# Kernel tuning notes

Hardware: AMD Instinct MI355X
Metric: run time of the kernel (lower is better)

Reference implementation:

```python
import jax, jax.numpy as jnp
import numpy as np

HEADS = 8
RANK = 4

def _lora(x, w_down, w_up, palette, in_dim, out_dim):
    # w_down: [RANK*in_dim, 15], w_up: [RANK*out_dim, 15], palette: [1, 15]
    down = (palette @ w_down.T).reshape(RANK, in_dim)   # [r, in]
    up = (palette @ w_up.T).reshape(out_dim, RANK)      # [out, r]
    return (x @ down.T) @ up.T                          # [..., out]


def setup_inputs() -> dict:
    key = jax.random.key(0)
    ks = jax.random.split(key, 16)
    B, S, D = 2, 2048, 1280
    def n(k, shape, std=0.02):
        return (jax.random.normal(k, shape, dtype=jnp.float32) * std).astype(jnp.float32)
    return {
        'hidden_states': jax.random.normal(ks[0], (B, S, D), dtype=jnp.float32),
        'color_palette': jax.random.uniform(ks[1], (1, 15), dtype=jnp.float32),
        'Wq': n(ks[2], (D, D)), 'Wk': n(ks[3], (D, D)),
        'Wv': n(ks[4], (D, D)), 'Wo': n(ks[5], (D, D)),
        'bo': jnp.zeros((D,), dtype=jnp.float32),
        'q_down': n(ks[6], (RANK * D, 15), 0.25), 'q_up': n(ks[7], (RANK * D, 15)),
        'k_down': n(ks[8], (RANK * D, 15), 0.25), 'k_up': n(ks[9], (RANK * D, 15)),
        'v_down': n(ks[10], (RANK * D, 15), 0.25), 'v_up': n(ks[11], (RANK * D, 15)),
        'o_down': n(ks[12], (RANK * D, 15), 0.25), 'o_up': n(ks[13], (RANK * D, 15)),
    }


def reference(hidden_states, color_palette, Wq, Wk, Wv, Wo, bo,
              q_down, q_up, k_down, k_up, v_down, v_up, o_down, o_up):
    B, S, D = hidden_states.shape
    H = HEADS
    hd = D // H
    scale = 1.0  # LoRA scale
    x = hidden_states
    # LoRA-augmented projections (self-attention: encoder_hidden_states = x)
    q = x @ Wq.T + scale * _lora(x, q_down, q_up, color_palette, D, D)
    k = x @ Wk.T + scale * _lora(x, k_down, k_up, color_palette, D, D)
    v = x @ Wv.T + scale * _lora(x, v_down, v_up, color_palette, D, D)
    # split heads: [B, S, D] -> [B, H, S, hd]
    q = q.reshape(B, S, H, hd).transpose(0, 2, 1, 3)
    k = k.reshape(B, S, H, hd).transpose(0, 2, 1, 3)
    v = v.reshape(B, S, H, hd).transpose(0, 2, 1, 3)
    attn_scale = 1.0 / jnp.sqrt(jnp.asarray(hd, dtype=q.dtype))
    scores = jnp.einsum('bhqd,bhkd->bhqk', q, k) * attn_scale
    probs = jax.nn.softmax(scores, axis=-1)
    out = jnp.einsum('bhqk,bhkd->bhqd', probs, v)
    out = out.transpose(0, 2, 1, 3).reshape(B, S, D)
    out = out @ Wo.T + bo + scale * _lora(out, o_down, o_up, color_palette, D, D)
    return out
```

## Files before the change

### kernel.cpp

```cpp
#include <hip/hip_runtime.h>

typedef unsigned short u16;
typedef unsigned int u32;
typedef __attribute__((ext_vector_type(4))) float floatx4;
typedef __attribute__((ext_vector_type(16))) float floatx16;
typedef __attribute__((ext_vector_type(8))) __bf16 bf16x8;
typedef __attribute__((ext_vector_type(2))) unsigned int u32x2;
typedef __attribute__((ext_vector_type(4))) unsigned int u32x4;

#define MFMA_BF16(a, b, c) __builtin_amdgcn_mfma_f32_16x16x32_bf16((a), (b), (c), 0, 0, 0)
#define MFMA32(a, b, c) __builtin_amdgcn_mfma_f32_32x32x16_bf16((a), (b), (c), 0, 0, 0)

typedef const __attribute__((address_space(1))) void* gas_ptr;
typedef __attribute__((address_space(3))) void* las_ptr;

__device__ __forceinline__ void gll16(const void* g, void* l) {
  __builtin_amdgcn_global_load_lds((gas_ptr)g, (las_ptr)l, 16, 0, 0);
}

__device__ __forceinline__ u16 f2bf(float x) {
  u32 u = __builtin_bit_cast(u32, x);
  u = (u + 0x7fffu + ((u >> 16) & 1u)) >> 16;
  return (u16)u;
}

__device__ __forceinline__ u32 cvtpk(float lo, float hi) {
  u32 r;
  asm("v_cvt_pk_bf16_f32 %0, %1, %2" : "=v"(r) : "v"(lo), "v"(hi));
  return r;
}

__global__ void prep_downup(const float* __restrict__ pal,
                            const float* __restrict__ qd, const float* __restrict__ qu,
                            const float* __restrict__ kd, const float* __restrict__ ku,
                            const float* __restrict__ vd, const float* __restrict__ vu,
                            const float* __restrict__ od, const float* __restrict__ ou,
                            float* __restrict__ down_f, float* __restrict__ up_f) {
  int tid = blockIdx.x * blockDim.x + threadIdx.x;
  int w = tid / 10240;
  int rem = tid - w * 10240;
  const float* dsrc = (w == 0) ? qd : (w == 1) ? kd : (w == 2) ? vd : od;
  const float* usrc = (w == 0) ? qu : (w == 1) ? ku : (w == 2) ? vu : ou;
  bool isdown = rem < 5120;
  int row = isdown ? rem : rem - 5120;
  const float* src = (isdown ? dsrc : usrc) + row * 15;
  float s = 0.f;
#pragma unroll
  for (int p = 0; p < 15; ++p) s += pal[p] * src[p];
  if (isdown) down_f[w * 5120 + row] = s;
  else        up_f[w * 5120 + row] = s;
}

__global__ void build_weff_cvtx(const float* __restrict__ Wq, const float* __restrict__ Wk,
                                const float* __restrict__ Wv, const float* __restrict__ Wo,
                                const float* __restrict__ down_f, const float* __restrict__ up_f,
                                u16* __restrict__ weff_qkv, u16* __restrict__ weff_o,
                                const float4* __restrict__ x, ushort4* __restrict__ xb) {
  if (blockIdx.x >= 25600) {
    int i = (blockIdx.x - 25600) * blockDim.x + threadIdx.x;
    float4 v = x[i];
    ushort4 o;
    o.x = f2bf(v.x); o.y = f2bf(v.y); o.z = f2bf(v.z); o.w = f2bf(v.w);
    xb[i] = o;
    return;
  }
  int tid = blockIdx.x * blockDim.x + threadIdx.x;
  int w = tid / 1638400;
  int rem = tid - w * 1638400;
  int n = rem / 1280;
  int k = rem - n * 1280;
  const float* W = (w == 0) ? Wq : (w == 1) ? Wk : (w == 2) ? Wv : Wo;
  const float* up = up_f + w * 5120 + n * 4;
  const float* dn = down_f + w * 5120 + k;
  float v = W[rem] + up[0] * dn[0] + up[1] * dn[1280] + up[2] * dn[2560] + up[3] * dn[3840];
  u16 hv = f2bf(v);
  if (w < 3) weff_qkv[w * 1638400 + rem] = hv;
  else       weff_o[rem] = hv;
}

__global__ __launch_bounds__(256) void gemm128_qkv(const u16* __restrict__ A, const u16* __restrict__ Bm,
                                                   u16* __restrict__ qb, u16* __restrict__ kb,
                                                   u16* __restrict__ vtb, int K) {
  __shared__ __align__(16) u16 smem[128 * 136];
  u16* lA = smem;
  u16* lB = smem + 8192;
  const int t = threadIdx.x;
  const int lane = t & 63;
  const int l15 = lane & 15, quad = lane >> 4;
  const int wid = t >> 6;
  const int wm = (wid >> 1) * 64;
  const int wn = (wid & 1) * 64;
  const int bm = blockIdx.x * 128;
  const int bn = blockIdx.y * 128;
  floatx4 acc[4][4] = {};

  int soff[4];
#pragma unroll
  for (int i = 0; i < 4; ++i) {
    int c = t + i * 256;
    int row = c >> 3, pos = c & 7;
    soff[i] = row * K + ((pos + row) & 7) * 8;
  }
  int afo[4][2], bfo[4][2];
#pragma unroll
  for (int i = 0; i < 4; ++i) {
#pragma unroll
    for (int ch = 0; ch < 2; ++ch) {
      int ra = wm + i * 16 + l15;
      int rb = wn + i * 16 + l15;
      int kc8 = ch * 4 + quad;
      afo[i][ch] = ra * 64 + ((kc8 - ra) & 7) * 8;
      bfo[i][ch] = rb * 64 + ((kc8 - rb) & 7) * 8;
    }
  }

  const u16* Ab = A + (long)bm * K;
  const u16* Bb = Bm + (long)bn * K;
  const int nkt = K >> 6;

  for (int kt = 0; kt < nkt; ++kt) {
    __syncthreads();
    const int k0 = kt * 64;
#pragma unroll
    for (int i = 0; i < 4; ++i) gll16(Ab + (long)soff[i] + k0, lA + (t + i * 256) * 8);
#pragma unroll
    for (int i = 0; i < 4; ++i) gll16(Bb + (long)soff[i] + k0, lB + (t + i * 256) * 8);
    __syncthreads();
#pragma unroll
    for (int ch = 0; ch < 2; ++ch) {
      bf16x8 af[4], bfr[4];
#pragma unroll
      for (int i = 0; i < 4; ++i) af[i] = *(const bf16x8*)(lA + afo[i][ch]);
#pragma unroll
      for (int i = 0; i < 4; ++i) bfr[i] = *(const bf16x8*)(lB + bfo[i][ch]);
#pragma unroll
      for (int i = 0; i < 4; ++i)
#pragma unroll
        for (int j = 0; j < 4; ++j)
          acc[i][j] = MFMA_BF16(af[i], bfr[j], acc[i][j]);
    }
  }

  if (bn < 2560) {
#pragma unroll
    for (int i = 0; i < 4; ++i) {
#pragma unroll
      for (int j = 0; j < 4; ++j) {
#pragma unroll
        for (int r = 0; r < 4; ++r) {
          int m = bm + wm + i * 16 + quad * 4 + r;
          int n = bn + wn + j * 16 + l15;
          u16 hv = f2bf(acc[i][j][r]);
          if (n < 1280) qb[(long)m * 1280 + n] = hv;
          else          kb[(long)m * 1280 + (n - 1280)] = hv;
        }
      }
    }
  } else {
    __syncthreads();
#pragma unroll
    for (int i = 0; i < 4; ++i)
#pragma unroll
      for (int j = 0; j < 4; ++j)
#pragma unroll
        for (int r = 0; r < 4; ++r) {
          int m_loc = wm + i * 16 + quad * 4 + r;
          int n_loc = wn + j * 16 + l15;
          smem[n_loc * 136 + m_loc] = f2bf(acc[i][j][r]);
        }
    __syncthreads();
    const int b = bm >> 11, sbase = bm & 2047;
    u16* dst = vtb + ((long)(b * 1280 + (bn - 2560))) * 2048 + sbase;
#pragma unroll
    for (int it = 0; it < 8; ++it) {
      int idx = it * 256 + t;
      int n_loc = idx >> 4;
      int m0 = (idx & 15) * 8;
      bf16x8 vv = *(const bf16x8*)(smem + n_loc * 136 + m0);
      *(bf16x8*)(dst + (long)n_loc * 2048 + m0) = vv;
    }
  }
}

__global__ __launch_bounds__(256) void gemm128_o(const u16* __restrict__ A, const u16* __restrict__ Bm,
                                                 float* __restrict__ outf,
                                                 const float* __restrict__ bias, int K) {
  __shared__ __align__(16) u16 lA[128 * 64];
  __shared__ __align__(16) u16 lB[128 * 64];
  const int t = threadIdx.x;
  const int lane = t & 63;
  const int l15 = lane & 15, quad = lane >> 4;
  const int wid = t >> 6;
  const int wm = (wid >> 1) * 64;
  const int wn = (wid & 1) * 64;
  const int bm = blockIdx.x * 128;
  const int bn = blockIdx.y * 128;
  floatx4 acc[4][4] = {};

  int soff[4];
#pragma unroll
  for (int i = 0; i < 4; ++i) {
    int c = t + i * 256;
    int row = c >> 3, pos = c & 7;
    soff[i] = row * K + ((pos + row) & 7) * 8;
  }
  int afo[4][2], bfo[4][2];
#pragma unroll
  for (int i = 0; i < 4; ++i) {
#pragma unroll
    for (int ch = 0; ch < 2; ++ch) {
      int ra = wm + i * 16 + l15;
      int rb = wn + i * 16 + l15;
      int kc8 = ch * 4 + quad;
      afo[i][ch] = ra * 64 + ((kc8 - ra) & 7) * 8;
      bfo[i][ch] = rb * 64 + ((kc8 - rb) & 7) * 8;
    }
  }

  const u16* Ab = A + (long)bm * K;
  const u16* Bb = Bm + (long)bn * K;
  const int nkt = K >> 6;

  for (int kt = 0; kt < nkt; ++kt) {
    __syncthreads();
    const int k0 = kt * 64;
#pragma unroll
    for (int i = 0; i < 4; ++i) gll16(Ab + (long)soff[i] + k0, lA + (t + i * 256) * 8);
#pragma unroll
    for (int i = 0; i < 4; ++i) gll16(Bb + (long)soff[i] + k0, lB + (t + i * 256) * 8);
    __syncthreads();
#pragma unroll
    for (int ch = 0; ch < 2; ++ch) {
      bf16x8 af[4], bfr[4];
#pragma unroll
      for (int i = 0; i < 4; ++i) af[i] = *(const bf16x8*)(lA + afo[i][ch]);
#pragma unroll
      for (int i = 0; i < 4; ++i) bfr[i] = *(const bf16x8*)(lB + bfo[i][ch]);
#pragma unroll
      for (int i = 0; i < 4; ++i)
#pragma unroll
        for (int j = 0; j < 4; ++j)
          acc[i][j] = MFMA_BF16(af[i], bfr[j], acc[i][j]);
    }
  }

#pragma unroll
  for (int i = 0; i < 4; ++i) {
#pragma unroll
    for (int j = 0; j < 4; ++j) {
#pragma unroll
      for (int r = 0; r < 4; ++r) {
        int m = bm + wm + i * 16 + quad * 4 + r;
        int n = bn + wn + j * 16 + l15;
        outf[(long)m * 1280 + n] = acc[i][j][r] + bias[n];
      }
    }
  }
}

__global__ __launch_bounds__(512) void flash_attn(const u16* __restrict__ qb,
                                                  const u16* __restrict__ kb,
                                                  const u16* __restrict__ vtb,
                                                  u16* __restrict__ attn) {
  const int D = 1280, HD = 160;
  __shared__ __align__(16) u16 kv_lds[2][20480];
  const int t = threadIdx.x, lane = t & 63, wid = t >> 6;
  const int l31 = lane & 31, hi = lane >> 5;
  const int rg = wid >> 1, kh = wid & 1;
  const int lflat = blockIdx.y * 16 + blockIdx.x;
  const int vswz = (lflat & 7) * 32 + (lflat >> 3);
  const int qi = vswz & 15, bh = vswz >> 4;
  const int b = bh >> 3, h = bh & 7;
  const int q0 = qi * 128 + rg * 32;
  const float kS = 0.11404582025f;

  bf16x8 aq[10];
  {
    const u16* qg = qb + ((long)(b * 2048 + q0 + l31)) * D + h * HD + hi * 8;
#pragma unroll
    for (int kw = 0; kw < 10; ++kw) aq[kw] = *(const bf16x8*)(qg + kw * 16);
  }

  const u16* sg[5];
  int sadv[5];
#pragma unroll
  for (int i = 0; i < 5; ++i) {
    int c = t + i * 512;
    if (c < 1280) {
      int key = c / 20, pos = c - key * 20;
      int g = pos - (3 * key) % 20;
      if (g < 0) g += 20;
      sg[i] = kb + ((long)(b * 2048 + key)) * D + h * HD + g * 8;
      sadv[i] = 64 * D;
    } else {
      int c2 = c - 1280;
      int vrow = c2 >> 3, swz = c2 & 7;
      int vcol = swz ^ (vrow & 7);
      sg[i] = vtb + ((long)(b * 1280 + h * HD + vrow)) * 2048 + vcol * 8;
      sadv[i] = 64;
    }
  }

  int kfo[10];
  {
    int key = kh * 32 + l31;
    int r3 = (3 * key) % 20;
#pragma unroll
    for (int kw = 0; kw < 10; ++kw) {
      int g = kw * 2 + hi;
      int pos = g + r3;
      if (pos >= 20) pos -= 20;
      kfo[kw] = (key * 20 + pos) * 8;
    }
  }
  int vfo[5][2];
#pragma unroll
  for (int db = 0; db < 5; ++db) {
#pragma unroll
    for (int w = 0; w < 2; ++w) {
      int d = db * 32 + l31;
      int gc = kh * 4 + w * 2 + hi;
      int sw = gc ^ (d & 7);
      vfo[db][w] = 10240 + (d * 8 + sw) * 8;
    }
  }

  float l_sum = 0.f;
  floatx16 o_acc[5] = {};
  bf16x8 paA = {}, paB = {};

  gll16(sg[0], &kv_lds[0][t * 8]);           sg[0] += sadv[0];
  gll16(sg[1], &kv_lds[0][(t + 512) * 8]);   sg[1] += sadv[1];
  if (wid < 4) { gll16(sg[2], &kv_lds[0][(t + 1024) * 8]); sg[2] += sadv[2]; }

  for (int kt0 = 0; kt0 < 32; ++kt0) {
    u16* kd = &kv_lds[(kt0 + 1) & 1][0];
    u16* vd = &kv_lds[kt0 & 1][0];
    if (kt0 < 31) {
      gll16(sg[0], kd + t * 8);          sg[0] += sadv[0];
      gll16(sg[1], kd + (t + 512) * 8);  sg[1] += sadv[1];
      if (wid < 4) { gll16(sg[2], kd + (t + 1024) * 8); sg[2] += sadv[2]; }
    }
    if (wid >= 4) { gll16(sg[2], vd + (t + 1024) * 8); sg[2] += sadv[2]; }
    gll16(sg[3], vd + (t + 1536) * 8);  sg[3] += sadv[3];
    gll16(sg[4], vd + (t + 2048) * 8);  sg[4] += sadv[4];

    if (kt0 < 31) asm volatile("s_waitcnt vmcnt(5)" ::: "memory");
    else          asm volatile("s_waitcnt vmcnt(0)" ::: "memory");
    __builtin_amdgcn_s_barrier();
    __builtin_amdgcn_sched_barrier(0);

    const u16* kbase = &kv_lds[kt0 & 1][0];
    const u16* vbase = &kv_lds[(kt0 + 1) & 1][0];

    floatx16 s0 = {}, s1 = {};
#pragma unroll
    for (int kw = 0; kw < 5; ++kw) {
      bf16x8 k0 = *(const bf16x8*)(kbase + kfo[kw * 2]);
      bf16x8 k1 = *(const bf16x8*)(kbase + kfo[kw * 2 + 1]);
      s0 = MFMA32(k0, aq[kw * 2], s0);
      s1 = MFMA32(k1, aq[kw * 2 + 1], s1);
    }

    if (kt0 > 0) {
#pragma unroll
      for (int db = 0; db < 5; ++db) {
        bf16x8 v0 = *(const bf16x8*)(vbase + vfo[db][0]);
        bf16x8 v1 = *(const bf16x8*)(vbase + vfo[db][1]);
        o_acc[db] = MFMA32(paA, v0, o_acc[db]);
        o_acc[db] = MFMA32(paB, v1, o_acc[db]);
      }
    }

    float p[16];
#pragma unroll
    for (int r = 0; r < 16; ++r) {
      p[r] = __builtin_exp2f(fminf((s0[r] + s1[r]) * kS, 80.f));
      l_sum += p[r];
    }
    u32 c01 = cvtpk(p[0], p[1]),  c23 = cvtpk(p[2], p[3]);
    u32 c45 = cvtpk(p[4], p[5]),  c67 = cvtpk(p[6], p[7]);
    u32 c89 = cvtpk(p[8], p[9]),  cAB = cvtpk(p[10], p[11]);
    u32 cCD = cvtpk(p[12], p[13]), cEF = cvtpk(p[14], p[15]);
    u32x2 r02 = __builtin_amdgcn_permlane32_swap(c01, c45, false, false);
    u32x2 r13 = __builtin_amdgcn_permlane32_swap(c23, c67, false, false);
    u32x2 r46 = __builtin_amdgcn_permlane32_swap(c89, cCD, false, false);
    u32x2 r57 = __builtin_amdgcn_permlane32_swap(cAB, cEF, false, false);
    u32x4 pk0 = {r02[0], r13[0], r02[1], r13[1]};
    u32x4 pk1 = {r46[0], r57[0], r46[1], r57[1]};
    paA = __builtin_bit_cast(bf16x8, pk0);
    paB = __builtin_bit_cast(bf16x8, pk1);

    __builtin_amdgcn_sched_barrier(0);
    __builtin_amdgcn_s_barrier();
  }

  {
    const u16* vbase = &kv_lds[1][0];
#pragma unroll
    for (int db = 0; db < 5; ++db) {
      bf16x8 v0 = *(const bf16x8*)(vbase + vfo[db][0]);
      bf16x8 v1 = *(const bf16x8*)(vbase + vfo[db][1]);
      o_acc[db] = MFMA32(paA, v0, o_acc[db]);
      o_acc[db] = MFMA32(paB, v1, o_acc[db]);
    }
  }
  __syncthreads();

  float* lscr = (float*)&kv_lds[0][0];
  lscr[wid * 64 + lane] = l_sum;
  __syncthreads();
  float rl[16];
#pragma unroll
  for (int r = 0; r < 16; ++r) {
    int q32 = (r & 3) + 8 * (r >> 2) + 4 * hi;
    float tot = lscr[(rg * 2 + 0) * 64 + q32] + lscr[(rg * 2 + 0) * 64 + q32 + 32]
              + lscr[(rg * 2 + 1) * 64 + q32] + lscr[(rg * 2 + 1) * 64 + q32 + 32];
    rl[r] = 1.0f / tot;
  }
  __syncthreads();
  float* oscr = (float*)&kv_lds[0][0];
  if (kh == 1) {
#pragma unroll
    for (int db = 0; db < 5; ++db)
#pragma unroll
      for (int r = 0; r < 16; ++r)
        oscr[rg * 5120 + (db * 16 + r) * 64 + lane] = o_acc[db][r];
  }
  __syncthreads();
  if (kh == 0) {
#pragma unroll
    for (int db = 0; db < 5; ++db) {
#pragma unroll
      for (int r = 0; r < 16; ++r) {
        float v = (o_acc[db][r] + oscr[rg * 5120 + (db * 16 + r) * 64 + lane]) * rl[r];
        int row = q0 + (r & 3) + 8 * (r >> 2) + 4 * hi;
        int col = h * HD + db * 32 + l31;
        attn[((long)(b * 2048 + row)) * D + col] = f2bf(v);
      }
    }
  }
}

extern "C" void kernel_launch(void* const* d_in, const int* in_sizes, int n_in,
                              void* d_out, int out_size, void* d_ws, size_t ws_size,
                              hipStream_t stream) {
  const float* x   = (const float*)d_in[0];
  const float* pal = (const float*)d_in[1];
  const float* Wq  = (const float*)d_in[2];
  const float* Wk  = (const float*)d_in[3];
  const float* Wv  = (const float*)d_in[4];
  const float* Wo  = (const float*)d_in[5];
  const float* bo  = (const float*)d_in[6];
  const float* qd  = (const float*)d_in[7];
  const float* qu  = (const float*)d_in[8];
  const float* kd  = (const float*)d_in[9];
  const float* ku  = (const float*)d_in[10];
  const float* vd  = (const float*)d_in[11];
  const float* vu  = (const float*)d_in[12];
  const float* od  = (const float*)d_in[13];
  const float* ou  = (const float*)d_in[14];
  float* out = (float*)d_out;

  char* ws = (char*)d_ws;
  u16* xb       = (u16*)(ws);
  u16* weff_qkv = (u16*)(ws + 10485760);
  u16* weff_o   = (u16*)(ws + 20316160);
  u16* qbuf     = (u16*)(ws + 23592960);
  u16* kbuf     = (u16*)(ws + 34078720);
  u16* vtb      = (u16*)(ws + 44564480);
  u16* attn     = (u16*)(ws + 55050240);
  float* down_f = (float*)(ws + 65536000);
  float* up_f   = (float*)(ws + 65617920);

  prep_downup<<<160, 256, 0, stream>>>(pal, qd, qu, kd, ku, vd, vu, od, ou, down_f, up_f);
  build_weff_cvtx<<<30720, 256, 0, stream>>>(Wq, Wk, Wv, Wo, down_f, up_f, weff_qkv, weff_o,
                                             (const float4*)x, (ushort4*)xb);
  gemm128_qkv<<<dim3(32, 30), 256, 0, stream>>>(xb, weff_qkv, qbuf, kbuf, vtb, 1280);
  flash_attn<<<dim3(16, 16), 512, 0, stream>>>(qbuf, kbuf, vtb, attn);
  gemm128_o<<<dim3(32, 10), 256, 0, stream>>>(attn, weff_o, out, bo, 1280);
}
```

Measured before the change: 267.6 us.

## Halve flash-attention block size and restructure K/V load schedule

```diff
diff --git a/kernel.cpp b/kernel.cpp
--- a/kernel.cpp
+++ b/kernel.cpp
@@ -258,20 +258,21 @@
   }
 }
 
-__global__ __launch_bounds__(512) void flash_attn(const u16* __restrict__ qb,
+__global__ __launch_bounds__(256) void flash_attn(const u16* __restrict__ qb,
                                                   const u16* __restrict__ kb,
                                                   const u16* __restrict__ vtb,
                                                   u16* __restrict__ attn) {
   const int D = 1280, HD = 160;
-  __shared__ __align__(16) u16 kv_lds[2][20480];
+  __shared__ __align__(16) u16 kbuf[2][10240];
+  __shared__ __align__(16) u16 vbuf_l[10240];
   const int t = threadIdx.x, lane = t & 63, wid = t >> 6;
   const int l31 = lane & 31, hi = lane >> 5;
   const int rg = wid >> 1, kh = wid & 1;
-  const int lflat = blockIdx.y * 16 + blockIdx.x;
-  const int vswz = (lflat & 7) * 32 + (lflat >> 3);
-  const int qi = vswz & 15, bh = vswz >> 4;
+  const int lflat = blockIdx.x;
+  const int vswz = (lflat & 7) * 64 + (lflat >> 3);
+  const int qi = vswz & 31, bh = vswz >> 5;
   const int b = bh >> 3, h = bh & 7;
-  const int q0 = qi * 128 + rg * 32;
+  const int q0 = qi * 64 + rg * 32;
   const float kS = 0.11404582025f;
 
   bf16x8 aq[10];
@@ -281,24 +282,22 @@
     for (int kw = 0; kw < 10; ++kw) aq[kw] = *(const bf16x8*)(qg + kw * 16);
   }
 
-  const u16* sg[5];
-  int sadv[5];
+  const u16* sgk[5];
 #pragma unroll
   for (int i = 0; i < 5; ++i) {
-    int c = t + i * 512;
-    if (c < 1280) {
-      int key = c / 20, pos = c - key * 20;
-      int g = pos - (3 * key) % 20;
-      if (g < 0) g += 20;
-      sg[i] = kb + ((long)(b * 2048 + key)) * D + h * HD + g * 8;
-      sadv[i] = 64 * D;
-    } else {
-      int c2 = c - 1280;
-      int vrow = c2 >> 3, swz = c2 & 7;
-      int vcol = swz ^ (vrow & 7);
-      sg[i] = vtb + ((long)(b * 1280 + h * HD + vrow)) * 2048 + vcol * 8;
-      sadv[i] = 64;
-    }
+    int c = t + i * 256;
+    int key = c / 20, pos = c - key * 20;
+    int g = pos - (3 * key) % 20;
+    if (g < 0) g += 20;
+    sgk[i] = kb + ((long)(b * 2048 + key)) * D + h * HD + g * 8;
+  }
+  const u16* sgv[5];
+#pragma unroll
+  for (int i = 0; i < 5; ++i) {
+    int c = t + i * 256;
+    int vrow = c >> 3, swz = c & 7;
+    int vcol = swz ^ (vrow & 7);
+    sgv[i] = vtb + ((long)(b * 1280 + h * HD + vrow)) * 2048 + vcol * 8;
   }
 
   int kfo[10];
@@ -321,38 +320,37 @@
       int d = db * 32 + l31;
       int gc = kh * 4 + w * 2 + hi;
       int sw = gc ^ (d & 7);
-      vfo[db][w] = 10240 + (d * 8 + sw) * 8;
+      vfo[db][w] = (d * 8 + sw) * 8;
     }
   }
 
   float l_sum = 0.f;
   floatx16 o_acc[5] = {};
-  bf16x8 paA = {}, paB = {};
-
-  gll16(sg[0], &kv_lds[0][t * 8]);           sg[0] += sadv[0];
-  gll16(sg[1], &kv_lds[0][(t + 512) * 8]);   sg[1] += sadv[1];
-  if (wid < 4) { gll16(sg[2], &kv_lds[0][(t + 1024) * 8]); sg[2] += sadv[2]; }
+
+#pragma unroll
+  for (int i = 0; i < 5; ++i) {
+    gll16(sgk[i], &kbuf[0][0] + (t + i * 256) * 8);
+    sgk[i] += 64 * D;
+  }
+  asm volatile("s_waitcnt vmcnt(0)" ::: "memory");
+  __builtin_amdgcn_s_barrier();
 
   for (int kt0 = 0; kt0 < 32; ++kt0) {
-    u16* kd = &kv_lds[(kt0 + 1) & 1][0];
-    u16* vd = &kv_lds[kt0 & 1][0];
+#pragma unroll
+    for (int i = 0; i < 5; ++i) {
+      gll16(sgv[i], &vbuf_l[0] + (t + i * 256) * 8);
+      sgv[i] += 64;
+    }
     if (kt0 < 31) {
-      gll16(sg[0], kd + t * 8);          sg[0] += sadv[0];
-      gll16(sg[1], kd + (t + 512) * 8);  sg[1] += sadv[1];
-      if (wid < 4) { gll16(sg[2], kd + (t + 1024) * 8); sg[2] += sadv[2]; }
-    }
-    if (wid >= 4) { gll16(sg[2], vd + (t + 1024) * 8); sg[2] += sadv[2]; }
-    gll16(sg[3], vd + (t + 1536) * 8);  sg[3] += sadv[3];
-    gll16(sg[4], vd + (t + 2048) * 8);  sg[4] += sadv[4];
-
-    if (kt0 < 31) asm volatile("s_waitcnt vmcnt(5)" ::: "memory");
-    else          asm volatile("s_waitcnt vmcnt(0)" ::: "memory");
-    __builtin_amdgcn_s_barrier();
-    __builtin_amdgcn_sched_barrier(0);
-
-    const u16* kbase = &kv_lds[kt0 & 1][0];
-    const u16* vbase = &kv_lds[(kt0 + 1) & 1][0];
-
+      u16* kd = &kbuf[(kt0 + 1) & 1][0];
+#pragma unroll
+      for (int i = 0; i < 5; ++i) {
+        gll16(sgk[i], kd + (t + i * 256) * 8);
+        sgk[i] += 64 * D;
+      }
+    }
+
+    const u16* kbase = &kbuf[kt0 & 1][0];
     floatx16 s0 = {}, s1 = {};
 #pragma unroll
     for (int kw = 0; kw < 5; ++kw) {
@@ -360,16 +358,6 @@
       bf16x8 k1 = *(const bf16x8*)(kbase + kfo[kw * 2 + 1]);
       s0 = MFMA32(k0, aq[kw * 2], s0);
       s1 = MFMA32(k1, aq[kw * 2 + 1], s1);
-    }
-
-    if (kt0 > 0) {
-#pragma unroll
-      for (int db = 0; db < 5; ++db) {
-        bf16x8 v0 = *(const bf16x8*)(vbase + vfo[db][0]);
-        bf16x8 v1 = *(const bf16x8*)(vbase + vfo[db][1]);
-        o_acc[db] = MFMA32(paA, v0, o_acc[db]);
-        o_acc[db] = MFMA32(paB, v1, o_acc[db]);
-      }
     }
 
     float p[16];
@@ -388,26 +376,28 @@
     u32x2 r57 = __builtin_amdgcn_permlane32_swap(cAB, cEF, false, false);
     u32x4 pk0 = {r02[0], r13[0], r02[1], r13[1]};
     u32x4 pk1 = {r46[0], r57[0], r46[1], r57[1]};
-    paA = __builtin_bit_cast(bf16x8, pk0);
-    paB = __builtin_bit_cast(bf16x8, pk1);
-
+    bf16x8 paA = __builtin_bit_cast(bf16x8, pk0);
+    bf16x8 paB = __builtin_bit_cast(bf16x8, pk1);
+
+    if (kt0 < 31) asm volatile("s_waitcnt vmcnt(5)" ::: "memory");
+    else          asm volatile("s_waitcnt vmcnt(0)" ::: "memory");
+    __builtin_amdgcn_s_barrier();
+    __builtin_amdgcn_sched_barrier(0);
+
+#pragma unroll
+    for (int db = 0; db < 5; ++db) {
+      bf16x8 v0 = *(const bf16x8*)(&vbuf_l[0] + vfo[db][0]);
+      bf16x8 v1 = *(const bf16x8*)(&vbuf_l[0] + vfo[db][1]);
+      o_acc[db] = MFMA32(paA, v0, o_acc[db]);
+      o_acc[db] = MFMA32(paB, v1, o_acc[db]);
+    }
+
+    asm volatile("s_waitcnt vmcnt(0)" ::: "memory");
     __builtin_amdgcn_sched_barrier(0);
     __builtin_amdgcn_s_barrier();
   }
 
-  {
-    const u16* vbase = &kv_lds[1][0];
-#pragma unroll
-    for (int db = 0; db < 5; ++db) {
-      bf16x8 v0 = *(const bf16x8*)(vbase + vfo[db][0]);
-      bf16x8 v1 = *(const bf16x8*)(vbase + vfo[db][1]);
-      o_acc[db] = MFMA32(paA, v0, o_acc[db]);
-      o_acc[db] = MFMA32(paB, v1, o_acc[db]);
-    }
-  }
-  __syncthreads();
-
-  float* lscr = (float*)&kv_lds[0][0];
+  float* lscr = (float*)&kbuf[0][0];
   lscr[wid * 64 + lane] = l_sum;
   __syncthreads();
   float rl[16];
@@ -419,7 +409,7 @@
     rl[r] = 1.0f / tot;
   }
   __syncthreads();
-  float* oscr = (float*)&kv_lds[0][0];
+  float* oscr = (float*)&kbuf[0][0];
   if (kh == 1) {
 #pragma unroll
     for (int db = 0; db < 5; ++db)
@@ -477,6 +467,6 @@
   build_weff_cvtx<<<30720, 256, 0, stream>>>(Wq, Wk, Wv, Wo, down_f, up_f, weff_qkv, weff_o,
                                              (const float4*)x, (ushort4*)xb);
   gemm128_qkv<<<dim3(32, 30), 256, 0, stream>>>(xb, weff_qkv, qbuf, kbuf, vtb, 1280);
-  flash_attn<<<dim3(16, 16), 512, 0, stream>>>(qbuf, kbuf, vtb, attn);
+  flash_attn<<<512, 256, 0, stream>>>(qbuf, kbuf, vtb, attn);
   gemm128_o<<<dim3(32, 10), 256, 0, stream>>>(attn, weff_o, out, bo, 1280);
 }
```

New measurement: 325.0 us. 1.21x slower.
